# Kernel tuning notes

Hardware: AMD Instinct MI355X
Metric: run time of the kernel (lower is better)

The kernel has to match this reference:

```python
import jax, jax.numpy as jnp
import numpy as np

D_MODEL = 1024
NHEAD = 16
HEAD_DIM = D_MODEL // NHEAD
B, S = 8, 1024
NEG = -1e9  # finite stand-in for -inf (same softmax result, grad-safe)


def setup_inputs() -> dict:
    key = jax.random.key(0)
    ks = jax.random.split(key, 12)
    sc = 1.0 / np.sqrt(D_MODEL)
    inp = {
        "q": jax.random.normal(ks[0], (B, S, D_MODEL), jnp.float32),
        "k": jax.random.normal(ks[1], (B, S, D_MODEL), jnp.float32),
        "v": jax.random.normal(ks[2], (B, S, D_MODEL), jnp.float32),
        "padding_mask": jax.random.bernoulli(ks[3], 0.1, (B, S)),
        "causal_mask": jnp.where(jnp.tril(jnp.ones((S, S), bool)), 0.0, NEG).astype(jnp.float32),
        "wq": jax.random.normal(ks[4], (D_MODEL, D_MODEL), jnp.float32) * sc,
        "bq": jax.random.normal(ks[5], (D_MODEL,), jnp.float32) * sc,
        "wk": jax.random.normal(ks[6], (D_MODEL, D_MODEL), jnp.float32) * sc,
        "wv": jax.random.normal(ks[7], (D_MODEL, D_MODEL), jnp.float32) * sc,
        "bv": jax.random.normal(ks[8], (D_MODEL,), jnp.float32) * sc,
        "wo": jax.random.normal(ks[9], (D_MODEL, D_MODEL), jnp.float32) * sc,
        "bo": jax.random.normal(ks[10], (D_MODEL,), jnp.float32) * sc,
    }
    return inp


def reference(q, k, v, padding_mask, causal_mask, wq, bq, wk, wv, bv, wo, bo):
    b = q.shape[0]
    # projections (torch Linear: x @ W.T + b); k_linear has no bias
    qp = q @ wq.T + bq
    kp = k @ wk.T
    vp = v @ wv.T + bv
    # [B, S, H, Dh] -> [B, H, S, Dh]
    qh = qp.reshape(b, -1, NHEAD, HEAD_DIM).transpose(0, 2, 1, 3)
    kh = kp.reshape(b, -1, NHEAD, HEAD_DIM).transpose(0, 2, 1, 3)
    vh = vp.reshape(b, -1, NHEAD, HEAD_DIM).transpose(0, 2, 1, 3)
    scores = jnp.einsum("bhqd,bhkd->bhqk", qh, kh) / np.sqrt(HEAD_DIM).astype(np.float32)
    scores = jnp.where(padding_mask[:, None, None, :], NEG, scores)
    scores = scores + causal_mask[None, None, :, :]
    attn = jax.nn.softmax(scores, axis=-1)
    out = jnp.einsum("bhqk,bhkd->bhqd", attn, vh)
    out = out.transpose(0, 2, 1, 3).reshape(b, -1, D_MODEL)
    return out @ wo.T + bo
```

## Files before the change

### kernel.cpp

```cpp
#include <hip/hip_runtime.h>
#include <hip/hip_bf16.h>
#include <cstdint>
#include <math.h>


typedef __bf16 bf16_t;
typedef __bf16 bf16x8 __attribute__((ext_vector_type(8)));
typedef __bf16 bf16x4 __attribute__((ext_vector_type(4)));
typedef float  f32x4  __attribute__((ext_vector_type(4)));

#define MFMA16(a, b, c) __builtin_amdgcn_mfma_f32_16x16x32_bf16((a), (b), (c), 0, 0, 0)
#define NEGV (-1e9f)

__device__ __forceinline__ void gl_lds16(const void* gp, void* lp) {
  __builtin_amdgcn_global_load_lds(
      (__attribute__((address_space(1))) void*)(gp),
      (__attribute__((address_space(3))) void*)(lp), 16, 0, 0);
}

__device__ __forceinline__ void bar() {
  asm volatile("" ::: "memory");
  __builtin_amdgcn_s_barrier();
  asm volatile("" ::: "memory");
}

__device__ __forceinline__ unsigned int pk2(float lo, float hi) {
  unsigned short a = __builtin_bit_cast(unsigned short, (bf16_t)lo);
  unsigned short b = __builtin_bit_cast(unsigned short, (bf16_t)hi);
  return (unsigned int)a | ((unsigned int)b << 16);
}

__device__ __forceinline__ void cvt_body(const float* __restrict__ in,
                                         bf16_t* __restrict__ out, int i) {
  const float4* p = reinterpret_cast<const float4*>(in) + (size_t)i * 2;
  float4 a = p[0], b = p[1];
  bf16x8 r = {(bf16_t)a.x, (bf16_t)a.y, (bf16_t)a.z, (bf16_t)a.w,
              (bf16_t)b.x, (bf16_t)b.y, (bf16_t)b.z, (bf16_t)b.w};
  *reinterpret_cast<bf16x8*>(out + (size_t)i * 8) = r;
}

__global__ __launch_bounds__(256) void cvt_w(
    const float* __restrict__ wq, const float* __restrict__ wk,
    const float* __restrict__ wv, const float* __restrict__ wo,
    bf16_t* __restrict__ owq, bf16_t* __restrict__ owk,
    bf16_t* __restrict__ owv, bf16_t* __restrict__ owo) {
  const int bid = (int)blockIdx.x;
  const int s = bid >> 9;
  const int i = (bid & 511) * 256 + (int)threadIdx.x;
  cvt_body(s == 0 ? wq : (s == 1 ? wk : (s == 2 ? wv : wo)),
           s == 0 ? owq : (s == 1 ? owk : (s == 2 ? owv : owo)), i);
}


struct AReg { float4 v[8]; };

__device__ __forceinline__ void loadA_f32(const float* __restrict__ Agf,
                                          int tile, AReg& g) {
  const size_t kt = (size_t)tile * 64;
#pragma unroll
  for (int rr = 0; rr < 4; rr++) {
    const float* src = Agf + (size_t)(rr * 64) * 1024 + kt;
    g.v[rr * 2]     = *(const float4*)(src);
    g.v[rr * 2 + 1] = *(const float4*)(src + 4);
  }
}

__device__ __forceinline__ void cvtWriteA(char* ldsA, int t, const AReg& g) {
#pragma unroll
  for (int rr = 0; rr < 4; rr++) {
    float4 a = g.v[rr * 2], b = g.v[rr * 2 + 1];
    bf16x8 r = {(bf16_t)a.x, (bf16_t)a.y, (bf16_t)a.z, (bf16_t)a.w,
                (bf16_t)b.x, (bf16_t)b.y, (bf16_t)b.z, (bf16_t)b.w};
    *(bf16x8*)(ldsA + rr * 8192 + t * 16) = r;
  }
}

__global__ __launch_bounds__(512) void gemm_qkv(const float* __restrict__ qf,
                                                const float* __restrict__ kf,
                                                const float* __restrict__ vf,
                                                const bf16_t* __restrict__ wqb,
                                                const bf16_t* __restrict__ wkb,
                                                const bf16_t* __restrict__ wvb,
                                                const float* __restrict__ bq,
                                                const float* __restrict__ bv,
                                                bf16_t* __restrict__ qp,
                                                bf16_t* __restrict__ kp,
                                                bf16_t* __restrict__ vtw) {
  __shared__ __align__(16) char lds[114688];
  const int bid = (int)blockIdx.x;
  const int z = bid >> 8;
  const int idx = bid & 255;
  const int p = ((idx >> 6) << 3) | (idx & 7);
  const int n = (idx >> 3) & 7;
  const float*  A = z == 0 ? qf : (z == 1 ? kf : vf);
  const bf16_t* W = z == 0 ? wqb : (z == 1 ? wkb : wvb);
  const int t = threadIdx.x;
  const int w = t >> 6, l = t & 63, lr = l & 15, lg = l >> 4;
  const int wr = w >> 1, wc = w & 1;
  const int m0 = p * 256, n0 = n * 128;
  const int K = 1024, N = 1024;

  const int gc = (t & 7) ^ ((t >> 3) & 7);
  const float*  Agf = A + (size_t)(m0 + (t >> 3)) * K + gc * 8;
  const bf16_t* Wg  = W + (size_t)(n0 + (t >> 3)) * K + gc * 8;

  auto stageB = [&](int buf, int tile) {
    char* dst = lds + 65536 + buf * 16384 + t * 16;
    const size_t kt = (size_t)tile * 64;
    gl_lds16(Wg + kt,                  dst);
    gl_lds16(Wg + kt + (size_t)64 * K, dst + 8192);
  };

  AReg g0, g1;
  loadA_f32(Agf, 0, g0);
  stageB(0, 0);
  loadA_f32(Agf, 1, g1);
  stageB(1, 1);
  asm volatile("s_waitcnt vmcnt(12)" ::: "memory");
  cvtWriteA(lds, t, g0);
  asm volatile("s_waitcnt vmcnt(10)" ::: "memory");
  asm volatile("s_waitcnt lgkmcnt(0)" ::: "memory");
  bar();

  f32x4 acc[4][4] = {};
  const int xorv = (lr & 7) << 4;
  const int k0o = lg * 16, k1o = 64 + lg * 16;

#define QKV_ITER(T, gIssue, gCvt)                                             \
  {                                                                           \
    const char* Ab = lds + ((T) & 1) * 32768;                                 \
    const char* Bb = lds + 65536 + ((T) % 3) * 16384;                         \
    bf16x8 af[4][2], b0[2][2], b1[2][2];                                      \
                              \
    _Pragma("unroll")                                                         \
    for (int mt = 0; mt < 4; mt++) {                                          \
      const int row = wr * 64 + mt * 16 + lr;                                 \
      af[mt][0] = *(const bf16x8*)(Ab + row * 128 + (k0o ^ xorv));            \
      af[mt][1] = *(const bf16x8*)(Ab + row * 128 + (k1o ^ xorv));            \
    }                                                                         \
    _Pragma("unroll")                                                         \
    for (int nt = 0; nt < 2; nt++) {                                          \
      const int row = wc * 64 + nt * 16 + lr;                                 \
      b0[nt][0] = *(const bf16x8*)(Bb + row * 128 + (k0o ^ xorv));            \
      b0[nt][1] = *(const bf16x8*)(Bb + row * 128 + (k1o ^ xorv));            \
    }                                                                         \
    if ((T) + 2 < 16) loadA_f32(Agf, (T) + 2, gIssue);                        \
    bar();                                                                    \
    asm volatile("s_waitcnt lgkmcnt(0)" ::: "memory");                        \
    __builtin_amdgcn_s_setprio(1);                                            \
    _Pragma("unroll")                                                         \
    for (int mt = 0; mt < 4; mt++)                                            \
      _Pragma("unroll")                                                       \
      for (int nt = 0; nt < 2; nt++) {                                        \
        acc[mt][nt] = MFMA16(af[mt][0], b0[nt][0], acc[mt][nt]);              \
        acc[mt][nt] = MFMA16(af[mt][1], b0[nt][1], acc[mt][nt]);              \
      }                                                                       \
    __builtin_amdgcn_s_setprio(0);                                            \
    bar();                                                                    \
       \
    _Pragma("unroll")                                                         \
    for (int nt = 0; nt < 2; nt++) {                                          \
      const int row = wc * 64 + (nt + 2) * 16 + lr;                           \
      b1[nt][0] = *(const bf16x8*)(Bb + row * 128 + (k0o ^ xorv));            \
      b1[nt][1] = *(const bf16x8*)(Bb + row * 128 + (k1o ^ xorv));            \
    }                                                                         \
    if ((T) + 2 < 16) stageB(((T) + 2) % 3, (T) + 2);                         \
    if ((T) < 14)       asm volatile("s_waitcnt vmcnt(10)" ::: "memory");     \
    else if ((T) == 14) asm volatile("s_waitcnt vmcnt(0)" ::: "memory");      \
    if ((T) + 1 < 16) cvtWriteA(lds + (((T) + 1) & 1) * 32768, t, gCvt);      \
    asm volatile("s_waitcnt lgkmcnt(0)" ::: "memory");                        \
    bar();                                                                    \
    __builtin_amdgcn_s_setprio(1);                                            \
    _Pragma("unroll")                                                         \
    for (int mt = 0; mt < 4; mt++)                                            \
      _Pragma("unroll")                                                       \
      for (int nt = 0; nt < 2; nt++) {                                        \
        acc[mt][nt + 2] = MFMA16(af[mt][0], b1[nt][0], acc[mt][nt + 2]);      \
        acc[mt][nt + 2] = MFMA16(af[mt][1], b1[nt][1], acc[mt][nt + 2]);      \
      }                                                                       \
    __builtin_amdgcn_s_setprio(0);                                            \
    bar();                                                                    \
  }

#pragma unroll 1
  for (int TT = 0; TT < 16; TT += 2) {
    QKV_ITER(TT, g0, g1)
    QKV_ITER(TT + 1, g1, g0)
  }
#undef QKV_ITER

  if (z != 2) {
    bf16_t* outp = (z == 0) ? qp : kp;
    const float sc = (z == 0) ? 0.125f : 1.0f;
#pragma unroll
    for (int nt = 0; nt < 4; nt++) {
      const int col = n0 + wc * 64 + nt * 16 + lr;
      const float bb = (z == 0) ? bq[col] : 0.0f;
#pragma unroll
      for (int mt = 0; mt < 4; mt++)
#pragma unroll
        for (int i = 0; i < 4; i++) {
          const int row = m0 + wr * 64 + mt * 16 + lg * 4 + i;
          outp[(size_t)row * N + col] = (bf16_t)((acc[mt][nt][i] + bb) * sc);
        }
    }
  } else {
    __syncthreads();
    char* Tl = lds;
#pragma unroll
    for (int nt = 0; nt < 4; nt++) {
      const int col_l = wc * 64 + nt * 16 + lr;
      const float bb = bv[n0 + col_l];
#pragma unroll
      for (int mt = 0; mt < 4; mt++)
#pragma unroll
        for (int i = 0; i < 4; i++) {
          const int row_l = wr * 64 + mt * 16 + lg * 4 + i;
          *(bf16_t*)(Tl + col_l * 512 + ((row_l * 2) ^ ((col_l & 7) << 4))) =
              (bf16_t)(acc[mt][nt][i] + bb);
        }
    }
    __syncthreads();
    const int b = m0 >> 10, s0 = m0 & 1023;
    const int c_l = t >> 2, sub = t & 3;
    bf16_t* dst = vtw + (size_t)(b * 1024 + n0 + c_l) * 1024 + s0 + sub * 64;
    const char* Trow = Tl + c_l * 512;
    const int sw2 = (c_l & 7) << 4;
#pragma unroll
    for (int jj = 0; jj < 8; jj++) {
      const int lc = sub * 8 + jj;
      bf16x8 vv = *(const bf16x8*)(Trow + ((lc << 4) ^ sw2));
      *(bf16x8*)(dst + jj * 8) = vv;
    }
  }
}

__global__ __launch_bounds__(512) void gemm_out(const bf16_t* __restrict__ A,
                                                const bf16_t* __restrict__ W,
                                                const float* __restrict__ bias,
                                                float* __restrict__ outp) {
  __shared__ __align__(16) char lds[147456];
  const int bid = (int)blockIdx.x;
  const int p = ((bid >> 6) << 3) | (bid & 7);
  const int n = (bid >> 3) & 7;
  const int t = threadIdx.x;
  const int w = t >> 6, l = t & 63, lr = l & 15, lg = l >> 4;
  const int wr = w >> 1, wc = w & 1;
  const int m0 = p * 256, n0 = n * 128;
  const int K = 1024, N = 1024;

  const int gc = (t & 7) ^ ((t >> 3) & 7);
  const bf16_t* Ag = A + (size_t)(m0 + (t >> 3)) * K + gc * 8;
  const bf16_t* Wg = W + (size_t)(n0 + (t >> 3)) * K + gc * 8;

  auto stageA = [&](int buf, int tile) {
    char* dst = lds + buf * 32768 + t * 16;
    const size_t kt = (size_t)tile * 64;
    gl_lds16(Ag + kt,                    dst);
    gl_lds16(Ag + kt + (size_t)64 * K,   dst + 8192);
    gl_lds16(Ag + kt + (size_t)128 * K,  dst + 16384);
    gl_lds16(Ag + kt + (size_t)192 * K,  dst + 24576);
  };
  auto stageB = [&](int buf, int tile) {
    char* dst = lds + 98304 + buf * 16384 + t * 16;
    const size_t kt = (size_t)tile * 64;
    gl_lds16(Wg + kt,                    dst);
    gl_lds16(Wg + kt + (size_t)64 * K,   dst + 8192);
  };
  stageA(0, 0); stageB(0, 0); stageA(1, 1); stageB(1, 1);
  asm volatile("s_waitcnt vmcnt(6)" ::: "memory");
  bar();

  f32x4 acc[4][4] = {};
  const int xorv = (lr & 7) << 4;
  const int k0o = lg * 16, k1o = 64 + lg * 16;

  for (int T = 0; T < 16; ++T) {
    const int cur = T % 3;
    const char* Ab = lds + cur * 32768;
    const char* Bb = lds + 98304 + cur * 16384;
    bf16x8 af[4][2], b0[2][2], b1[2][2];
#pragma unroll
    for (int mt = 0; mt < 4; mt++) {
      const int row = wr * 64 + mt * 16 + lr;
      af[mt][0] = *(const bf16x8*)(Ab + row * 128 + (k0o ^ xorv));
      af[mt][1] = *(const bf16x8*)(Ab + row * 128 + (k1o ^ xorv));
    }
#pragma unroll
    for (int nt = 0; nt < 2; nt++) {
      const int row = wc * 64 + nt * 16 + lr;
      b0[nt][0] = *(const bf16x8*)(Bb + row * 128 + (k0o ^ xorv));
      b0[nt][1] = *(const bf16x8*)(Bb + row * 128 + (k1o ^ xorv));
    }
    if (T + 2 < 16) stageA((T + 2) % 3, T + 2);
    bar();
    asm volatile("s_waitcnt lgkmcnt(0)" ::: "memory");
    __builtin_amdgcn_s_setprio(1);
#pragma unroll
    for (int mt = 0; mt < 4; mt++)
#pragma unroll
      for (int nt = 0; nt < 2; nt++) {
        acc[mt][nt] = MFMA16(af[mt][0], b0[nt][0], acc[mt][nt]);
        acc[mt][nt] = MFMA16(af[mt][1], b0[nt][1], acc[mt][nt]);
      }
    __builtin_amdgcn_s_setprio(0);
    bar();
#pragma unroll
    for (int nt = 0; nt < 2; nt++) {
      const int row = wc * 64 + (nt + 2) * 16 + lr;
      b1[nt][0] = *(const bf16x8*)(Bb + row * 128 + (k0o ^ xorv));
      b1[nt][1] = *(const bf16x8*)(Bb + row * 128 + (k1o ^ xorv));
    }
    if (T + 2 < 16) stageB((T + 2) % 3, T + 2);
    if (T < 14)       asm volatile("s_waitcnt vmcnt(6)" ::: "memory");
    else if (T == 14) asm volatile("s_waitcnt vmcnt(0)" ::: "memory");
    bar();
    asm volatile("s_waitcnt lgkmcnt(0)" ::: "memory");
    __builtin_amdgcn_s_setprio(1);
#pragma unroll
    for (int mt = 0; mt < 4; mt++)
#pragma unroll
      for (int nt = 0; nt < 2; nt++) {
        acc[mt][nt + 2] = MFMA16(af[mt][0], b1[nt][0], acc[mt][nt + 2]);
        acc[mt][nt + 2] = MFMA16(af[mt][1], b1[nt][1], acc[mt][nt + 2]);
      }
    __builtin_amdgcn_s_setprio(0);
    bar();
  }

#pragma unroll
  for (int nt = 0; nt < 4; nt++) {
    const int col = n0 + wc * 64 + nt * 16 + lr;
    const float bb = bias[col];
#pragma unroll
    for (int mt = 0; mt < 4; mt++)
#pragma unroll
      for (int i = 0; i < 4; i++) {
        const int row = m0 + wr * 64 + mt * 16 + lg * 4 + i;
        outp[(size_t)row * N + col] = acc[mt][nt][i] + bb;
      }
  }
}

__device__ __forceinline__ void pack_bfly(const f32x4 (&s)[4], int lg,
                                          bf16x8& pbv0, bf16x8& pbv1) {
  unsigned int u[4][2], sh[4][2];
#pragma unroll
  for (int nt = 0; nt < 4; nt++) {
    u[nt][0] = pk2(s[nt][0], s[nt][1]);
    u[nt][1] = pk2(s[nt][2], s[nt][3]);
  }
#pragma unroll
  for (int nt = 0; nt < 4; nt++) {
    sh[nt][0] = (unsigned int)__shfl_xor((int)u[nt][0], 16, 64);
    sh[nt][1] = (unsigned int)__shfl_xor((int)u[nt][1], 16, 64);
  }
  const bool ev = (lg & 1) == 0;
  unsigned int Y[8];
  Y[0] = ev ? u[0][0] : sh[1][0];  Y[1] = ev ? u[0][1] : sh[1][1];
  Y[2] = ev ? u[2][0] : sh[3][0];  Y[3] = ev ? u[2][1] : sh[3][1];
  Y[4] = ev ? sh[0][0] : u[1][0];  Y[5] = ev ? sh[0][1] : u[1][1];
  Y[6] = ev ? sh[2][0] : u[3][0];  Y[7] = ev ? sh[2][1] : u[3][1];
  const bool mid = (lg == 1) || (lg == 2);
#pragma unroll
  for (int j = 0; j < 8; j++) {
    const unsigned int z = (unsigned int)__shfl_xor((int)Y[j], 48, 64);
    Y[j] = mid ? z : Y[j];
  }
  union U8 { unsigned int u[4]; bf16x8 v; };
  U8 p0, p1;
  p0.u[0] = Y[0]; p0.u[1] = Y[1]; p0.u[2] = Y[4]; p0.u[3] = Y[5];
  p1.u[0] = Y[2]; p1.u[1] = Y[3]; p1.u[2] = Y[6]; p1.u[3] = Y[7];
  pbv0 = p0.v;
  pbv1 = p1.v;
}

__global__ __launch_bounds__(512, 8) void attn_fused(const bf16_t* __restrict__ qp,
                                                     const bf16_t* __restrict__ kp,
                                                     const bf16_t* __restrict__ vt,
                                                     const int* __restrict__ pad,
                                                     bf16_t* __restrict__ outp) {
  __shared__ bf16_t Ks[2][64 * 64];
  __shared__ bf16_t Vts[2][64 * 64];
  __shared__ int padI[1024];
  __shared__ int sfl[8], sfh[8];
  const int t = threadIdx.x, w = t >> 6, l = t & 63, lr = l & 15, lg = l >> 4;
  const int L = (int)blockIdx.x;
  const int bh = (L & 7) + ((L >> 6) << 3);
  const int j = (L >> 3) & 7;
  const int b = bh >> 4, h = bh & 15;
  const int lo = j, hi = 15 - j;

  const int srow = t >> 3, sc = t & 7;
  const int gc = sc ^ (srow & 7);
  const bf16_t* kgb = kp + (size_t)(b * 1024 + srow) * 1024 + h * 64 + gc * 8;
  const bf16_t* vgb = vt + (size_t)(bh * 64 + srow) * 1024 + gc * 8;

  auto stage = [&](int bufi, int k0s) {
    gl_lds16(kgb + (size_t)k0s * 1024, (char*)(Ks[bufi]) + t * 16);
    gl_lds16(vgb + k0s,                (char*)(Vts[bufi]) + t * 16);
  };

  bool unl = false, unh = false;
  for (int jj = t; jj <= hi * 64; jj += 512) {
    const bool u = (pad[b * 1024 + jj] == 0);
    unh |= u;
    unl |= (u && (jj <= lo * 64));
  }
  const bool al = __any(unl), ah = __any(unh);
  if (l == 0) { sfl[w] = al ? 1 : 0; sfh[w] = ah ? 1 : 0; }

  stage(0, 0);
  if (t < 256) gl_lds16(pad + b * 1024 + t * 4, (char*)padI + t * 16);

  const int mytile = (w < 4) ? hi : lo;
  const int qrow_l = mytile * 64 + (w & 3) * 16 + lr;
  const int base16 = mytile * 64 + (w & 3) * 16;
  const bf16_t* qg = qp + (size_t)(b * 1024 + qrow_l) * 1024 + h * 64 + lg * 8;
  const bf16x8 qa0 = *reinterpret_cast<const bf16x8*>(qg);
  const bf16x8 qa1 = *reinterpret_cast<const bf16x8*>(qg + 32);

  __syncthreads();
  int ul = 0, uh = 0;
#pragma unroll
  for (int i = 0; i < 8; i++) { ul |= sfl[i]; uh |= sfh[i]; }
  const bool mydeg = (w < 4) ? (uh == 0) : (ul == 0);
  const int ktEnd = (ul == 0) ? 16 : (hi + 1);

  f32x4 o[4] = {};
  float m_ = -INFINITY, ld_ = 0.0f;

  for (int kt = 0; kt < ktEnd; ++kt) {
    const int cur = kt & 1;
    if (kt + 1 < ktEnd) {
      stage(cur ^ 1, (kt + 1) * 64);
      asm volatile("s_waitcnt vmcnt(2)" ::: "memory");
    } else {
      asm volatile("s_waitcnt vmcnt(0)" ::: "memory");
    }
    __builtin_amdgcn_s_barrier();

    if (kt <= mytile || mydeg) {
      const char* Kb = (const char*)(Ks[cur]);
      const char* Vb = (const char*)(Vts[cur]);
      const int k0 = kt * 64;

      f32x4 s[4] = {};
#pragma unroll
      for (int nt = 0; nt < 4; nt++) {
        const int row = nt * 16 + lr;
        const int sw = (row & 7) << 4;
        bf16x8 kb0 = *reinterpret_cast<const bf16x8*>(Kb + row * 128 + ((lg * 16) ^ sw));
        bf16x8 kb1 = *reinterpret_cast<const bf16x8*>(Kb + row * 128 + ((lg * 16 + 64) ^ sw));
        s[nt] = MFMA16(kb0, qa0, s[nt]);
        s[nt] = MFMA16(kb1, qa1, s[nt]);
      }

      const bool nc = (k0 + 63 > base16);
#pragma unroll
      for (int nt = 0; nt < 4; nt++) {
        const int kc4 = k0 + nt * 16 + lg * 4;
        const int4 pd = *reinterpret_cast<const int4*>(&padI[kc4]);
        const int pdv[4] = {pd.x, pd.y, pd.z, pd.w};
#pragma unroll
        for (int i = 0; i < 4; i++) {
          float v = s[nt][i];
          if (pdv[i]) v = NEGV;
          if (nc && (kc4 + i > qrow_l)) v += NEGV;
          s[nt][i] = v;
        }
      }

      float mx = s[0][0];
#pragma unroll
      for (int nt = 0; nt < 4; nt++)
#pragma unroll
        for (int i = 0; i < 4; i++) mx = fmaxf(mx, s[nt][i]);
      mx = fmaxf(mx, __shfl_xor(mx, 16, 64));
      mx = fmaxf(mx, __shfl_xor(mx, 32, 64));

      if (!__all(mx <= m_ - 88.0f)) {
        if (!__all(mx <= m_ + 8.0f)) {
          const float mn = fmaxf(m_, mx);
          const float scl = __expf(m_ - mn);
          m_ = mn;
          ld_ *= scl;
#pragma unroll
          for (int nt = 0; nt < 4; nt++) o[nt] *= scl;
        }
        float a = 0.0f;
#pragma unroll
        for (int nt = 0; nt < 4; nt++)
#pragma unroll
          for (int i = 0; i < 4; i++) {
            const float p = __expf(s[nt][i] - m_);
            s[nt][i] = p;
            a += p;
          }
        a += __shfl_xor(a, 16, 64);
        a += __shfl_xor(a, 32, 64);
        ld_ += a;

        bf16x8 pb0, pb1;
        pack_bfly(s, lg, pb0, pb1);

#pragma unroll
        for (int nt = 0; nt < 4; nt++) {
          const int vrow = nt * 16 + lr;
          const int vsw = (vrow & 7) << 4;
          bf16x8 vf0 = *reinterpret_cast<const bf16x8*>(Vb + vrow * 128 + ((lg * 16) ^ vsw));
          bf16x8 vf1 = *reinterpret_cast<const bf16x8*>(Vb + vrow * 128 + ((64 + lg * 16) ^ vsw));
          o[nt] = MFMA16(vf0, pb0, o[nt]);
          o[nt] = MFMA16(vf1, pb1, o[nt]);
        }
      }
    }
    __builtin_amdgcn_s_barrier();
  }

  const float rinv = 1.0f / ld_;
#pragma unroll
  for (int nt = 0; nt < 4; nt++) {
    bf16x4 rr = {(bf16_t)(o[nt][0] * rinv), (bf16_t)(o[nt][1] * rinv),
                 (bf16_t)(o[nt][2] * rinv), (bf16_t)(o[nt][3] * rinv)};
    *reinterpret_cast<bf16x4*>(outp + (size_t)(b * 1024 + qrow_l) * 1024 + h * 64 + nt * 16 + lg * 4) = rr;
  }
}

extern "C" void kernel_launch(void* const* d_in, const int* in_sizes, int n_in,
                              void* d_out, int out_size, void* d_ws, size_t ws_size,
                              hipStream_t stream) {
  const float* q   = (const float*)d_in[0];
  const float* k   = (const float*)d_in[1];
  const float* v   = (const float*)d_in[2];
  const int*   pad = (const int*)d_in[3];
  const float* wq  = (const float*)d_in[5];
  const float* bq  = (const float*)d_in[6];
  const float* wk  = (const float*)d_in[7];
  const float* wv  = (const float*)d_in[8];
  const float* bv  = (const float*)d_in[9];
  const float* wo  = (const float*)d_in[10];
  const float* bo  = (const float*)d_in[11];

  char* ws = (char*)d_ws;
  const size_t MiB = 1024 * 1024;
  bf16_t* attnO = (bf16_t*)(ws + 0 * MiB);
  bf16_t* qp  = (bf16_t*)(ws + 48 * MiB);
  bf16_t* kp  = (bf16_t*)(ws + 64 * MiB);
  bf16_t* vtw = (bf16_t*)(ws + 80 * MiB);
  bf16_t* wqb = (bf16_t*)(ws + 96 * MiB);
  bf16_t* wkb = (bf16_t*)(ws + 98 * MiB);
  bf16_t* wvb = (bf16_t*)(ws + 100 * MiB);
  bf16_t* wob = (bf16_t*)(ws + 102 * MiB);

  cvt_w<<<2048, 256, 0, stream>>>(wq, wk, wv, wo, wqb, wkb, wvb, wob);

  gemm_qkv<<<768, 512, 0, stream>>>(q, k, v, wqb, wkb, wvb, bq, bv, qp, kp, vtw);

  attn_fused<<<1024, 512, 0, stream>>>(qp, kp, vtw, pad, attnO);

  gemm_out<<<256, 512, 0, stream>>>(attnO, wob, bo, (float*)d_out);
}
```

Baseline: 191.1 us.

## Pre-convert QKV activations to bf16 and stream both GEMM operands via direct LDS loads

Activation conversion from fp32 to bf16 moves out of the QKV GEMM into a combined conversion kernel that also handles the weights. The GEMM then loads both A and B tiles with global_load_lds in a three-stage pipeline over 32-wide k tiles. It uses less LDS and declares launch bounds for higher occupancy. This drops the per-iteration register staging and conversion inside the GEMM. The cost is an extra full read and write pass over the 3x32MB activations in a separate kernel, and the attention output buffer now aliases the bf16 q buffer.

Measured after the change: 171.4 us. -10.3%, faster.

```diff
diff --git a/kernel.cpp b/kernel.cpp
--- a/kernel.cpp
+++ b/kernel.cpp
@@ -39,60 +39,46 @@
   *reinterpret_cast<bf16x8*>(out + (size_t)i * 8) = r;
 }
 
-__global__ __launch_bounds__(256) void cvt_w(
+__global__ __launch_bounds__(256) void cvt_all(
+    const float* __restrict__ q, const float* __restrict__ k, const float* __restrict__ v,
     const float* __restrict__ wq, const float* __restrict__ wk,
     const float* __restrict__ wv, const float* __restrict__ wo,
+    bf16_t* __restrict__ oq, bf16_t* __restrict__ ok, bf16_t* __restrict__ ov,
     bf16_t* __restrict__ owq, bf16_t* __restrict__ owk,
     bf16_t* __restrict__ owv, bf16_t* __restrict__ owo) {
   const int bid = (int)blockIdx.x;
-  const int s = bid >> 9;
-  const int i = (bid & 511) * 256 + (int)threadIdx.x;
-  cvt_body(s == 0 ? wq : (s == 1 ? wk : (s == 2 ? wv : wo)),
-           s == 0 ? owq : (s == 1 ? owk : (s == 2 ? owv : owo)), i);
-}
-
-
-struct AReg { float4 v[8]; };
-
-__device__ __forceinline__ void loadA_f32(const float* __restrict__ Agf,
-                                          int tile, AReg& g) {
-  const size_t kt = (size_t)tile * 64;
-#pragma unroll
-  for (int rr = 0; rr < 4; rr++) {
-    const float* src = Agf + (size_t)(rr * 64) * 1024 + kt;
-    g.v[rr * 2]     = *(const float4*)(src);
-    g.v[rr * 2 + 1] = *(const float4*)(src + 4);
-  }
-}
-
-__device__ __forceinline__ void cvtWriteA(char* ldsA, int t, const AReg& g) {
-#pragma unroll
-  for (int rr = 0; rr < 4; rr++) {
-    float4 a = g.v[rr * 2], b = g.v[rr * 2 + 1];
-    bf16x8 r = {(bf16_t)a.x, (bf16_t)a.y, (bf16_t)a.z, (bf16_t)a.w,
-                (bf16_t)b.x, (bf16_t)b.y, (bf16_t)b.z, (bf16_t)b.w};
-    *(bf16x8*)(ldsA + rr * 8192 + t * 16) = r;
-  }
-}
-
-__global__ __launch_bounds__(512) void gemm_qkv(const float* __restrict__ qf,
-                                                const float* __restrict__ kf,
-                                                const float* __restrict__ vf,
-                                                const bf16_t* __restrict__ wqb,
-                                                const bf16_t* __restrict__ wkb,
-                                                const bf16_t* __restrict__ wvb,
-                                                const float* __restrict__ bq,
-                                                const float* __restrict__ bv,
-                                                bf16_t* __restrict__ qp,
-                                                bf16_t* __restrict__ kp,
-                                                bf16_t* __restrict__ vtw) {
-  __shared__ __align__(16) char lds[114688];
+  if (bid < 12288) {
+    const int s = bid >> 12;
+    const int i = (bid & 4095) * 256 + (int)threadIdx.x;
+    cvt_body(s == 0 ? q : (s == 1 ? k : v),
+             s == 0 ? oq : (s == 1 ? ok : ov), i);
+  } else {
+    const int r = bid - 12288;
+    const int s = r >> 9;
+    const int i = (r & 511) * 256 + (int)threadIdx.x;
+    cvt_body(s == 0 ? wq : (s == 1 ? wk : (s == 2 ? wv : wo)),
+             s == 0 ? owq : (s == 1 ? owk : (s == 2 ? owv : owo)), i);
+  }
+}
+
+__global__ __launch_bounds__(512, 4) void gemm_qkv(const bf16_t* __restrict__ qbf,
+                                                   const bf16_t* __restrict__ kbf,
+                                                   const bf16_t* __restrict__ vbf,
+                                                   const bf16_t* __restrict__ wqb,
+                                                   const bf16_t* __restrict__ wkb,
+                                                   const bf16_t* __restrict__ wvb,
+                                                   const float* __restrict__ bq,
+                                                   const float* __restrict__ bv,
+                                                   bf16_t* __restrict__ qp,
+                                                   bf16_t* __restrict__ kp,
+                                                   bf16_t* __restrict__ vtw) {
+  __shared__ __align__(16) char lds[73728];
   const int bid = (int)blockIdx.x;
   const int z = bid >> 8;
   const int idx = bid & 255;
   const int p = ((idx >> 6) << 3) | (idx & 7);
   const int n = (idx >> 3) & 7;
-  const float*  A = z == 0 ? qf : (z == 1 ? kf : vf);
+  const bf16_t* A = z == 0 ? qbf : (z == 1 ? kbf : vbf);
   const bf16_t* W = z == 0 ? wqb : (z == 1 ? wkb : wvb);
   const int t = threadIdx.x;
   const int w = t >> 6, l = t & 63, lr = l & 15, lg = l >> 4;
@@ -100,94 +86,52 @@
   const int m0 = p * 256, n0 = n * 128;
   const int K = 1024, N = 1024;
 
-  const int gc = (t & 7) ^ ((t >> 3) & 7);
-  const float*  Agf = A + (size_t)(m0 + (t >> 3)) * K + gc * 8;
-  const bf16_t* Wg  = W + (size_t)(n0 + (t >> 3)) * K + gc * 8;
-
+  const int gc = (t & 3) ^ ((t >> 3) & 3);
+  const bf16_t* Ag = A + (size_t)(m0 + (t >> 2)) * K + gc * 8;
+  const bf16_t* Wg = W + (size_t)(n0 + (t >> 2)) * K + gc * 8;
+
+  auto stageA = [&](int buf, int tile) {
+    char* dst = lds + buf * 16384 + t * 16;
+    const size_t kt = (size_t)tile * 32;
+    gl_lds16(Ag + kt,                   dst);
+    gl_lds16(Ag + kt + (size_t)128 * K, dst + 8192);
+  };
   auto stageB = [&](int buf, int tile) {
-    char* dst = lds + 65536 + buf * 16384 + t * 16;
-    const size_t kt = (size_t)tile * 64;
-    gl_lds16(Wg + kt,                  dst);
-    gl_lds16(Wg + kt + (size_t)64 * K, dst + 8192);
+    gl_lds16(Wg + (size_t)tile * 32, lds + 49152 + buf * 8192 + t * 16);
   };
 
-  AReg g0, g1;
-  loadA_f32(Agf, 0, g0);
-  stageB(0, 0);
-  loadA_f32(Agf, 1, g1);
-  stageB(1, 1);
-  asm volatile("s_waitcnt vmcnt(12)" ::: "memory");
-  cvtWriteA(lds, t, g0);
-  asm volatile("s_waitcnt vmcnt(10)" ::: "memory");
-  asm volatile("s_waitcnt lgkmcnt(0)" ::: "memory");
+  stageA(0, 0); stageB(0, 0); stageA(1, 1); stageB(1, 1);
+  asm volatile("s_waitcnt vmcnt(3)" ::: "memory");
   bar();
 
   f32x4 acc[4][4] = {};
-  const int xorv = (lr & 7) << 4;
-  const int k0o = lg * 16, k1o = 64 + lg * 16;
-
-#define QKV_ITER(T, gIssue, gCvt)                                             \
-  {                                                                           \
-    const char* Ab = lds + ((T) & 1) * 32768;                                 \
-    const char* Bb = lds + 65536 + ((T) % 3) * 16384;                         \
-    bf16x8 af[4][2], b0[2][2], b1[2][2];                                      \
-                              \
-    _Pragma("unroll")                                                         \
-    for (int mt = 0; mt < 4; mt++) {                                          \
-      const int row = wr * 64 + mt * 16 + lr;                                 \
-      af[mt][0] = *(const bf16x8*)(Ab + row * 128 + (k0o ^ xorv));            \
-      af[mt][1] = *(const bf16x8*)(Ab + row * 128 + (k1o ^ xorv));            \
-    }                                                                         \
-    _Pragma("unroll")                                                         \
-    for (int nt = 0; nt < 2; nt++) {                                          \
-      const int row = wc * 64 + nt * 16 + lr;                                 \
-      b0[nt][0] = *(const bf16x8*)(Bb + row * 128 + (k0o ^ xorv));            \
-      b0[nt][1] = *(const bf16x8*)(Bb + row * 128 + (k1o ^ xorv));            \
-    }                                                                         \
-    if ((T) + 2 < 16) loadA_f32(Agf, (T) + 2, gIssue);                        \
-    bar();                                                                    \
-    asm volatile("s_waitcnt lgkmcnt(0)" ::: "memory");                        \
-    __builtin_amdgcn_s_setprio(1);                                            \
-    _Pragma("unroll")                                                         \
-    for (int mt = 0; mt < 4; mt++)                                            \
-      _Pragma("unroll")                                                       \
-      for (int nt = 0; nt < 2; nt++) {                                        \
-        acc[mt][nt] = MFMA16(af[mt][0], b0[nt][0], acc[mt][nt]);              \
-        acc[mt][nt] = MFMA16(af[mt][1], b0[nt][1], acc[mt][nt]);              \
-      }                                                                       \
-    __builtin_amdgcn_s_setprio(0);                                            \
-    bar();                                                                    \
-       \
-    _Pragma("unroll")                                                         \
-    for (int nt = 0; nt < 2; nt++) {                                          \
-      const int row = wc * 64 + (nt + 2) * 16 + lr;                           \
-      b1[nt][0] = *(const bf16x8*)(Bb + row * 128 + (k0o ^ xorv));            \
-      b1[nt][1] = *(const bf16x8*)(Bb + row * 128 + (k1o ^ xorv));            \
-    }                                                                         \
-    if ((T) + 2 < 16) stageB(((T) + 2) % 3, (T) + 2);                         \
-    if ((T) < 14)       asm volatile("s_waitcnt vmcnt(10)" ::: "memory");     \
-    else if ((T) == 14) asm volatile("s_waitcnt vmcnt(0)" ::: "memory");      \
-    if ((T) + 1 < 16) cvtWriteA(lds + (((T) + 1) & 1) * 32768, t, gCvt);      \
-    asm volatile("s_waitcnt lgkmcnt(0)" ::: "memory");                        \
-    bar();                                                                    \
-    __builtin_amdgcn_s_setprio(1);                                            \
-    _Pragma("unroll")                                                         \
-    for (int mt = 0; mt < 4; mt++)                                            \
-      _Pragma("unroll")                                                       \
-      for (int nt = 0; nt < 2; nt++) {                                        \
-        acc[mt][nt + 2] = MFMA16(af[mt][0], b1[nt][0], acc[mt][nt + 2]);      \
-        acc[mt][nt + 2] = MFMA16(af[mt][1], b1[nt][1], acc[mt][nt + 2]);      \
-      }                                                                       \
-    __builtin_amdgcn_s_setprio(0);                                            \
-    bar();                                                                    \
-  }
-
-#pragma unroll 1
-  for (int TT = 0; TT < 16; TT += 2) {
-    QKV_ITER(TT, g0, g1)
-    QKV_ITER(TT + 1, g1, g0)
-  }
-#undef QKV_ITER
+  const int cofs = (lg ^ ((lr >> 1) & 3)) << 4;
+
+  for (int T = 0; T < 32; ++T) {
+    const int cur = T % 3;
+    const char* Ab = lds + cur * 16384;
+    const char* Bb = lds + 49152 + cur * 8192;
+    bf16x8 af[4], bfr[4];
+#pragma unroll
+    for (int mt = 0; mt < 4; mt++)
+      af[mt] = *(const bf16x8*)(Ab + (wr * 64 + mt * 16 + lr) * 64 + cofs);
+#pragma unroll
+    for (int nt = 0; nt < 4; nt++)
+      bfr[nt] = *(const bf16x8*)(Bb + (wc * 64 + nt * 16 + lr) * 64 + cofs);
+    if (T + 2 < 32) { stageA((T + 2) % 3, T + 2); stageB((T + 2) % 3, T + 2); }
+    if (T < 30)       asm volatile("s_waitcnt vmcnt(3)" ::: "memory");
+    else if (T == 30) asm volatile("s_waitcnt vmcnt(0)" ::: "memory");
+    bar();
+    asm volatile("s_waitcnt lgkmcnt(0)" ::: "memory");
+    __builtin_amdgcn_s_setprio(1);
+#pragma unroll
+    for (int mt = 0; mt < 4; mt++)
+#pragma unroll
+      for (int nt = 0; nt < 4; nt++)
+        acc[mt][nt] = MFMA16(af[mt], bfr[nt], acc[mt][nt]);
+    __builtin_amdgcn_s_setprio(0);
+    bar();
+  }
 
   if (z != 2) {
     bf16_t* outp = (z == 0) ? qp : kp;
@@ -544,7 +488,9 @@
 
   char* ws = (char*)d_ws;
   const size_t MiB = 1024 * 1024;
-  bf16_t* attnO = (bf16_t*)(ws + 0 * MiB);
+  bf16_t* qbf = (bf16_t*)(ws + 0 * MiB);
+  bf16_t* kbf = (bf16_t*)(ws + 16 * MiB);
+  bf16_t* vbf = (bf16_t*)(ws + 32 * MiB);
   bf16_t* qp  = (bf16_t*)(ws + 48 * MiB);
   bf16_t* kp  = (bf16_t*)(ws + 64 * MiB);
   bf16_t* vtw = (bf16_t*)(ws + 80 * MiB);
@@ -552,10 +498,12 @@
   bf16_t* wkb = (bf16_t*)(ws + 98 * MiB);
   bf16_t* wvb = (bf16_t*)(ws + 100 * MiB);
   bf16_t* wob = (bf16_t*)(ws + 102 * MiB);
-
-  cvt_w<<<2048, 256, 0, stream>>>(wq, wk, wv, wo, wqb, wkb, wvb, wob);
-
-  gemm_qkv<<<768, 512, 0, stream>>>(q, k, v, wqb, wkb, wvb, bq, bv, qp, kp, vtw);
+  bf16_t* attnO = qbf;
+
+  cvt_all<<<14336, 256, 0, stream>>>(q, k, v, wq, wk, wv, wo,
+                                     qbf, kbf, vbf, wqb, wkb, wvb, wob);
+
+  gemm_qkv<<<768, 512, 0, stream>>>(qbf, kbf, vbf, wqb, wkb, wvb, bq, bv, qp, kp, vtw);
 
   attn_fused<<<1024, 512, 0, stream>>>(qp, kp, vtw, pad, attnO);
 
```
